# Optimization experiments

Measured on AMD Instinct MI355X. Metric: run time of the kernel, lower is better.

Reference implementation:

```python
import jax, jax.numpy as jnp
import numpy as np
from jax import lax

K_NEIGH = 20
BN_EPS = 1e-5


def conv2d(x, w, b, pad):
    # x: [B,C,H,W], w: [O,I,kh,kw]
    y = lax.conv_general_dilated(x, w, (1, 1), [(pad, pad), (pad, pad)],
                                 dimension_numbers=('NCHW', 'OIHW', 'NCHW'))
    return y + b[None, :, None, None]


def bn_train(h, gamma, beta):
    # h: [B,N,K,C]; BatchNorm1d in train mode: stats over (B,N,K) per channel
    mean = jnp.mean(h, axis=(0, 1, 2), keepdims=True)
    var = jnp.mean(jnp.square(h - mean), axis=(0, 1, 2), keepdims=True)
    return gamma * (h - mean) * lax.rsqrt(var + BN_EPS) + beta


def edge_conv(F1, w1, b1, g1, bt1, w2, b2, g2, bt2):
    # F1: [B,N,F] with F=1
    B, N, Fd = F1.shape
    sq = jnp.sum(F1 * F1, axis=-1)                               # [B,N]
    dist = sq[:, :, None] + sq[:, None, :] - 2.0 * jnp.einsum('bnf,bmf->bnm', F1, F1)
    idx = jnp.argsort(dist, axis=-1)[:, :, 1:K_NEIGH + 1]        # [B,N,K]
    knn = jax.vmap(lambda xb, ib: xb[ib])(F1, idx)               # [B,N,K,F]
    x1 = jnp.broadcast_to(F1[:, :, None, :], (B, N, K_NEIGH, Fd))
    x_in = jnp.concatenate([x1, knn - x1], axis=-1)              # [B,N,K,2F]
    h = jnp.einsum('bnkc,oc->bnko', x_in, w1) + b1               # 1x1 conv1d
    h = jax.nn.relu(bn_train(h, g1, bt1))
    o = jnp.einsum('bnkc,oc->bnko', h, w2) + b2
    o = jax.nn.relu(bn_train(o, g2, bt2))
    return jnp.max(o, axis=2)                                    # [B,N,an]


def pixel_shuffle(x, r):
    B, C, H, W = x.shape
    x = x.reshape(B, C // (r * r), r, r, H, W)
    x = x.transpose(0, 1, 4, 2, 5, 3)
    return x.reshape(B, C // (r * r), H * r, W * r)


def setup_inputs() -> dict:
    key = jax.random.key(0)
    ks = jax.random.split(key, 8)
    B, H, W = 4, 64, 64
    inp = {
        'x':   jax.random.normal(ks[0], (B, 1, H, W), jnp.float32),
        'c1w': jax.random.normal(ks[1], (64, 1, 5, 5), jnp.float32) * 0.1,
        'c1b': jnp.zeros((64,), jnp.float32),
        'c2w': jax.random.normal(ks[2], (32, 64, 3, 3), jnp.float32) * 0.05,
        'c2b': jnp.zeros((32,), jnp.float32),
        'c3w': jax.random.normal(ks[3], (16, 32, 3, 3), jnp.float32) * 0.05,
        'c3b': jnp.zeros((16,), jnp.float32),
        'c4w': jax.random.normal(ks[4], (1, 16, 3, 3), jnp.float32) * 0.05,
        'c4b': jnp.zeros((1,), jnp.float32),
        'ew1': jax.random.normal(ks[5], (3, 16, 2), jnp.float32) * 0.5,
        'eb1': jnp.zeros((3, 16), jnp.float32),
        'eg1': jnp.ones((3, 16), jnp.float32),
        'ebt1': jnp.zeros((3, 16), jnp.float32),
        'ew2': jax.random.normal(ks[6], (3, 1, 16), jnp.float32) * 0.25,
        'eb2': jnp.zeros((3, 1), jnp.float32),
        'eg2': jnp.ones((3, 1), jnp.float32),
        'ebt2': jnp.zeros((3, 1), jnp.float32),
    }
    return inp


def reference(x, c1w, c1b, c2w, c2b, c3w, c3b, c4w, c4b,
              ew1, eb1, eg1, ebt1, ew2, eb2, eg2, ebt2):
    h = jnp.tanh(conv2d(x, c1w, c1b, 2))
    h = jnp.tanh(conv2d(h, c2w, c2b, 1))
    h = jnp.tanh(conv2d(h, c3w, c3b, 1))
    h = conv2d(h, c4w, c4b, 1)                     # [B,1,H,W]
    B, C, H, W = h.shape
    F1 = h.reshape(B, C, H * W).transpose(0, 2, 1)  # [B,N,1]
    branches = [h]
    for i in range(3):
        o = edge_conv(F1, ew1[i], eb1[i], eg1[i], ebt1[i],
                      ew2[i], eb2[i], eg2[i], ebt2[i])  # [B,N,1]
        branches.append(o.transpose(0, 2, 1).reshape(B, C, H, W))
    p = jnp.concatenate(branches, axis=1)          # [B,4,H,W]
    return jax.nn.sigmoid(pixel_shuffle(p, 2))     # [B,1,2H,2W]
```

## Files before the change

### kernel.cpp

```cpp
#include <hip/hip_runtime.h>
#include <math.h>

#define NPIX 4096
#define KN 20
#define MTOT 327680.0

__device__ inline unsigned long long shflx64(unsigned long long v, int m) {
  unsigned lo = (unsigned)v, hi = (unsigned)(v >> 32);
  lo = __shfl_xor(lo, m, 64);
  hi = __shfl_xor(hi, m, 64);
  return (((unsigned long long)hi) << 32) | lo;
}

__global__ __launch_bounds__(512) void conv12_k(const float* __restrict__ x,
    const float* __restrict__ c1w, const float* __restrict__ c1b,
    const float* __restrict__ c2w, const float* __restrict__ c2b,
    float* __restrict__ part12) {
  __shared__ float sx[506];
  __shared__ float sc1[5472];
  const int tid = threadIdx.x;
  const int b = blockIdx.x, tile = blockIdx.y, z = blockIdx.z;
  const int th = (tile >> 2) << 4, tw = (tile & 3) << 4;

  for (int i = tid; i < 484; i += 512) {
    int r = i / 22, c = i - r*22;
    int gr = th - 3 + r, gc = tw - 3 + c;
    sx[r*23 + c] = (gr>=0 && gr<64 && gc>=0 && gc<64) ? x[b*NPIX + (gr<<6) + gc] : 0.f;
  }
  __syncthreads();
  for (int idx = tid; idx < 5184; idx += 512) {
    int co = idx / 324, rem = idx - co*324;
    int i = rem / 18, j = rem - i*18;
    int gy = th - 1 + i, gx = tw - 1 + j;
    bool inb = (gy>=0 && gy<64 && gx>=0 && gx<64);
    int cg = (z << 4) + co;
    float acc = c1b[cg];
#pragma unroll
    for (int di=0; di<5; di++)
#pragma unroll
      for (int dj=0; dj<5; dj++)
        acc = fmaf(sx[(i+di)*23 + j+dj], c1w[cg*25 + di*5 + dj], acc);
    sc1[co*342 + i*19 + j] = inb ? tanhf(acc) : 0.f;
  }
  __syncthreads();
  {
    const int l = tid & 63;
    const int w = __builtin_amdgcn_readfirstlane(tid >> 6);
    int row0 = (l >> 4) << 2;
    int col  = l & 15;
    int co0 = w << 2;
    float acc[16];
#pragma unroll
    for (int p=0;p<4;p++)
#pragma unroll
      for (int q=0;q<4;q++)
        acc[p*4+q] = (z == 0) ? c2b[co0+q] : 0.f;
#pragma unroll 2
    for (int ci = 0; ci < 16; ci++) {
      const float* sp = sc1 + ci*342;
      float vb[6][3];
#pragma unroll
      for (int r=0;r<6;r++)
#pragma unroll
        for (int dj=0;dj<3;dj++)
          vb[r][dj] = sp[(row0+r)*19 + col + dj];
      int cin = (z << 4) + ci;
#pragma unroll
      for (int q=0;q<4;q++) {
        const float* wq = c2w + ((size_t)(co0+q)*64 + cin)*9;
#pragma unroll
        for (int p=0;p<4;p++) {
          float a = acc[p*4+q];
#pragma unroll
          for (int di=0;di<3;di++)
#pragma unroll
            for (int dj=0;dj<3;dj++)
              a = fmaf(vb[p+di][dj], wq[di*3+dj], a);
          acc[p*4+q] = a;
        }
      }
    }
#pragma unroll
    for (int q=0;q<4;q++)
#pragma unroll
      for (int p=0;p<4;p++)
        part12[(((size_t)(z*4 + b)*32 + co0+q) << 12)
               + ((th+row0+p)<<6) + tw + col] = acc[p*4+q];
  }
}

__global__ __launch_bounds__(512) void conv34_k(const float* __restrict__ part12,
    const float* __restrict__ c3w, const float* __restrict__ c3b,
    const float* __restrict__ c4w, const float* __restrict__ c4b,
    float* __restrict__ fbuf) {
  __shared__ float sc2[3328];
  __shared__ float sc3[1248];
  __shared__ float red[1200];
  const int tid = threadIdx.x;
  const int b = blockIdx.x, tile = blockIdx.y;
  const int th = (tile >> 3) << 2, tw = (tile & 7) << 3;
  const int px = tid & 127;
  const int cinw = __builtin_amdgcn_readfirstlane(tid >> 7);

  for (int i = tid; i < 3072; i += 512) {
    int cin = i / 96, rem = i - cin*96;
    int rr = rem / 12, cc = rem - rr*12;
    int gr = th - 2 + rr, gc = tw - 2 + cc;
    float v = 0.f;
    if (gr>=0 && gr<64 && gc>=0 && gc<64) {
      size_t idx = (((size_t)b*32 + cin) << 12) + (gr<<6) + gc;
      v = tanhf(part12[idx] + part12[idx + 524288] +
                part12[idx + 1048576] + part12[idx + 1572864]);
    }
    sc2[cin*104 + rr*13 + cc] = v;
  }
  __syncthreads();
  float acc[16];
  int pi = px / 10, pj = px - pi*10;
  if (px < 60) {
#pragma unroll
    for (int o=0;o<16;o++) acc[o] = (cinw == 0) ? c3b[o] : 0.f;
    for (int ci = 0; ci < 8; ci++) {
      int cin = (cinw << 3) + ci;
      const float* sp = sc2 + cin*104;
      float v[9];
#pragma unroll
      for (int di=0;di<3;di++)
#pragma unroll
        for (int dj=0;dj<3;dj++)
          v[di*3+dj] = sp[(pi+di)*13 + pj+dj];
      const float* wc = c3w + cin*9;
#pragma unroll
      for (int o=0;o<16;o++) {
        const float* wo = wc + o*288;
#pragma unroll
        for (int t=0;t<9;t++)
          acc[o] = fmaf(v[t], wo[t], acc[o]);
      }
    }
  }
  int gy = th - 1 + pi, gx = tw - 1 + pj;
  bool inb = (gy>=0 && gy<64 && gx>=0 && gx<64);
  for (int ch = 0; ch < 4; ch++) {
    __syncthreads();
    if (px < 60) {
#pragma unroll
      for (int cc = 0; cc < 4; cc++)
        red[cinw*300 + px*5 + cc] = acc[(ch<<2) + cc];
    }
    __syncthreads();
    if (px < 60) {
      float s = red[0*300 + px*5 + cinw];
#pragma unroll
      for (int g=1; g<4; g++) s += red[g*300 + px*5 + cinw];
      int co = (ch<<2) + cinw;
      sc3[co*78 + pi*13 + pj] = inb ? tanhf(s) : 0.f;
    }
  }
  __syncthreads();
  if (tid < 32) {
    int py = tid >> 3, qx = tid & 7;
    float acc4 = c4b[0];
    for (int cin = 0; cin < 16; cin++) {
#pragma unroll
      for (int di=0;di<3;di++)
#pragma unroll
        for (int dj=0;dj<3;dj++)
          acc4 = fmaf(sc3[cin*78 + (py+di)*13 + qx+dj], c4w[cin*9 + di*3+dj], acc4);
    }
    fbuf[b*NPIX + ((th+py)<<6) + (tw+qx)] = acc4;
  }
}

__global__ __launch_bounds__(1024) void sort2_k(const float* __restrict__ f,
    float* __restrict__ sval, int* __restrict__ sidx) {
  int b = blockIdx.x;
  int tid = threadIdx.x;
  int l = tid & 63, w = tid >> 6;
  __shared__ unsigned long long Ab[NPIX];
  __shared__ unsigned long long Bb[NPIX];
  const float* fb = f + b*NPIX;
  unsigned long long key[4];
#pragma unroll
  for (int r=0;r<4;r++) {
    unsigned e = (w<<8) + (r<<6) + l;
    float v = fb[e];
    unsigned u = __float_as_uint(v);
    u ^= (u >> 31) ? 0xFFFFFFFFu : 0x80000000u;
    key[r] = (((unsigned long long)u) << 32) | e;
  }
  for (unsigned k = 2; k <= 256; k <<= 1) {
    for (unsigned j = k >> 1; j > 0; j >>= 1) {
      if (j >= 64) {
        unsigned rj = j >> 6;
#pragma unroll
        for (int r=0;r<4;r++) {
          int pr = r ^ (int)rj;
          if (pr > r) {
            unsigned e = (w<<8)+((unsigned)r<<6)+l;
            bool up = ((e & k & 255u) == 0);
            unsigned long long a = key[r], c = key[pr];
            bool sw = up ? (c < a) : (c > a);
            if (sw) { key[r] = c; key[pr] = a; }
          }
        }
      } else {
#pragma unroll
        for (int r=0;r<4;r++) {
          unsigned e = (w<<8)+((unsigned)r<<6)+l;
          unsigned long long a = key[r];
          unsigned long long p = shflx64(a, (int)j);
          bool up = ((e & k & 255u) == 0);
          bool keepmin = ((e & j) == 0) == up;
          key[r] = (keepmin ? (p < a) : (p > a)) ? p : a;
        }
      }
    }
  }
#pragma unroll
  for (int r=0;r<4;r++) Ab[(w<<8)+(r<<6)+l] = key[r];
  __syncthreads();
  unsigned long long* src = Ab;
  unsigned long long* dst = Bb;
  for (int lg = 8; lg <= 11; lg++) {
    const int L = 1 << lg;
    int p0 = tid << 2;
    int ri = p0 >> lg;
    int base = (ri ^ 1) << lg;
    int mbase = ((ri >> 1) << (lg + 1)) + (p0 & (L - 1));
    unsigned long long kk[4];
    int lo[4], hi[4];
#pragma unroll
    for (int r=0;r<4;r++) { kk[r] = src[p0 + r]; lo[r] = 0; hi[r] = L; }
    for (int s = 0; s <= lg; s++) {
#pragma unroll
      for (int r=0;r<4;r++) {
        if (lo[r] < hi[r]) {
          int mid = (lo[r] + hi[r]) >> 1;
          if (src[base + mid] < kk[r]) lo[r] = mid + 1; else hi[r] = mid;
        }
      }
    }
#pragma unroll
    for (int r=0;r<4;r++) dst[mbase + r + lo[r]] = kk[r];
    __syncthreads();
    unsigned long long* t = src; src = dst; dst = t;
  }
#pragma unroll
  for (int r=0;r<4;r++) {
    int p = (tid << 2) + r;
    unsigned long long kk = src[p];
    unsigned u = (unsigned)(kk >> 32);
    u ^= (u >> 31) ? 0x80000000u : 0xFFFFFFFFu;
    sval[b*NPIX + p] = __uint_as_float(u);
    sidx[b*NPIX + p] = (int)(kk & 0xFFFFFFFFu);
  }
}

__global__ __launch_bounds__(512) void knn4_k(const float* __restrict__ f,
    const float* __restrict__ sval, const int* __restrict__ sidx,
    float* __restrict__ dout, double* __restrict__ part1) {
  const int tid = threadIdx.x, blk = blockIdx.x;
  const int l = tid & 63, w = tid >> 6;
  const int bq = blk >> 7;
  const float* svb = sval + (bq << 12);
  const int*   sib = sidx + (bq << 12);
  const float* fB  = f + (bq << 12);
  double a0=0, a1=0, a2=0, a3=0, a4=0;
  unsigned long long kk[4];
  float fnp[4];
  int   sp[4];
#pragma unroll
  for (int p=0;p<4;p++) {
    int s = ((blk & 127) << 5) + (w << 2) + p;
    sp[p] = s;
    float fn = svb[s]; fnp[p] = fn;
    int start = s - 32;
    if (start < 0) start = 0;
    if (start > NPIX - 64) start = NPIX - 64;
    int q = start + l;
    float fm = svb[q];
    int   m  = sib[q];
    float sqn = __fmul_rn(fn, fn);
    float pr  = __fmul_rn(fn, fm);
    float dist = __fsub_rn(__fadd_rn(sqn, __fmul_rn(fm, fm)), __fmul_rn(2.0f, pr));
    unsigned u = __float_as_uint(dist);
    u ^= (u >> 31) ? 0xFFFFFFFFu : 0x80000000u;
    kk[p] = (((unsigned long long)u) << 32) | (unsigned)m;
  }
#pragma unroll
  for (int k = 2; k <= 64; k <<= 1)
#pragma unroll
    for (int j = k >> 1; j > 0; j >>= 1) {
#pragma unroll
      for (int p=0;p<4;p++) {
        unsigned long long pp = shflx64(kk[p], j);
        bool up = ((l & k) == 0);
        bool keepmin = ((l & j) == 0) == up;
        kk[p] = (keepmin ? (pp < kk[p]) : (pp > kk[p])) ? pp : kk[p];
      }
    }
#pragma unroll
  for (int p=0;p<4;p++) {
    int mr = (int)(kk[p] & 0xFFFFFFFFu);
    float fn = fnp[p];
    float d = __fsub_rn(fB[mr], fn);
    int n = sib[sp[p]];
    if (l >= 1 && l <= 20)
      dout[(size_t)((bq<<12) + n)*KN + (l-1)] = d;
    float dm = (l >= 1 && l <= 20) ? d : 0.f;
    a2 += (double)dm;
    a3 += (double)dm * (double)dm;
    a4 += (double)fn * (double)dm;
    if (l == 0) { a0 += (double)fn; a1 += (double)fn * (double)fn; }
  }
  double v[5] = {a0, a1, a2, a3, a4};
#pragma unroll
  for (int qi=0; qi<5; qi++)
    for (int off=32; off>0; off>>=1) v[qi] += __shfl_down(v[qi], off, 64);
  __shared__ double sred[8][5];
  if (l == 0)
#pragma unroll
    for (int qi=0; qi<5; qi++) sred[w][qi] = v[qi];
  __syncthreads();
  if (tid == 0) {
#pragma unroll
    for (int qi=0; qi<5; qi++) {
      double s = 0.0;
#pragma unroll
      for (int ww=0; ww<8; ww++) s += sred[ww][qi];
      part1[blk*5 + qi] = s;
    }
  }
}

__global__ __launch_bounds__(64) void branch_k(const float* __restrict__ f,
    const float* __restrict__ dw, const double* __restrict__ part1,
    const float* __restrict__ ew1, const float* __restrict__ eb1,
    const float* __restrict__ eg1, const float* __restrict__ ebt1,
    const float* __restrict__ ew2, const float* __restrict__ eb2,
    float* __restrict__ maxo, float* __restrict__ mino,
    double* __restrict__ part2) {
  const int l = threadIdx.x;
  const int blk = blockIdx.x, br = blockIdx.y;
  double a[5] = {0,0,0,0,0};
  for (int b2 = l; b2 < 512; b2 += 64)
#pragma unroll
    for (int q=0;q<5;q++) a[q] += part1[b2*5+q];
#pragma unroll
  for (int q=0;q<5;q++)
    for (int off=32; off>0; off>>=1) a[q] += __shfl_down(a[q], off, 64);
#pragma unroll
  for (int q=0;q<5;q++) a[q] = __shfl(a[q], 0, 64);
  double Ef = a[0]/16384.0, Eff = a[1]/16384.0;
  double Ed = a[2]/MTOT, Edd = a[3]/MTOT, Efd = a[4]/MTOT;
  double Vf = Eff - Ef*Ef, Vd = Edd - Ed*Ed, Cfd = Efd - Ef*Ed;
  float sA[16], sB[16], sC[16], sW[16];
#pragma unroll
  for (int c=0;c<16;c++) {
    int idx = br*16 + c;
    double w0 = (double)ew1[idx*2+0], w1 = (double)ew1[idx*2+1];
    double b1 = (double)eb1[idx];
    double m1 = w0*Ef + w1*Ed + b1;
    double v1 = w0*w0*Vf + 2.0*w0*w1*Cfd + w1*w1*Vd;
    double r1 = 1.0 / sqrt(v1 + 1e-5);
    double g = (double)eg1[idx];
    sA[c] = (float)(g*r1*w0);
    sB[c] = (float)(g*r1*w1);
    sC[c] = (float)(g*r1*(b1 - m1) + (double)ebt1[idx]);
    sW[c] = ew2[idx];
  }
  int row = (blk << 6) + l;
  float fv = f[row];
  const float* dd = dw + (size_t)row*KN;
  float b2v = eb2[br];
  float P[16];
#pragma unroll
  for (int c=0;c<16;c++) P[c] = fmaf(sA[c], fv, sC[c]);
  float mx = -INFINITY, mn = INFINITY;
  double s = 0.0, s2 = 0.0;
  for (int k=0;k<KN;k++) {
    float d = dd[k];
    float t = b2v;
#pragma unroll
    for (int c=0;c<16;c++)
      t = fmaf(sW[c], fmaxf(fmaf(sB[c], d, P[c]), 0.f), t);
    mx = fmaxf(mx, t);
    mn = fminf(mn, t);
    double td = (double)t;
    s += td; s2 += td*td;
  }
  maxo[br*16384 + row] = mx;
  mino[br*16384 + row] = mn;
#pragma unroll
  for (int off=32; off>0; off>>=1) {
    s  += __shfl_down(s, off, 64);
    s2 += __shfl_down(s2, off, 64);
  }
  if (l == 0) {
    part2[(br*256 + blk)*2 + 0] = s;
    part2[(br*256 + blk)*2 + 1] = s2;
  }
}

__global__ __launch_bounds__(256) void out_k(const float* __restrict__ f,
    const float* __restrict__ maxo, const float* __restrict__ mino,
    const double* __restrict__ part2,
    const float* __restrict__ eg2, const float* __restrict__ ebt2,
    float* __restrict__ out) {
  __shared__ float c2c[3][2];
  const int tid = threadIdx.x, blk = blockIdx.x;
  const int l = tid & 63, w = tid >> 6;
  if (w < 3) {
    int br = w;
    double s = 0.0, s2 = 0.0;
#pragma unroll
    for (int i=0;i<4;i++) {
      int bb = l + (i << 6);
      s  += part2[(br*256 + bb)*2 + 0];
      s2 += part2[(br*256 + bb)*2 + 1];
    }
#pragma unroll
    for (int off=32; off>0; off>>=1) {
      s  += __shfl_down(s, off, 64);
      s2 += __shfl_down(s2, off, 64);
    }
    if (l == 0) {
      double mean = s / MTOT;
      double var = s2 / MTOT - mean*mean;
      double r2 = 1.0 / sqrt(var + 1e-5);
      double sc = (double)eg2[br] * r2;
      c2c[br][0] = (float)sc;
      c2c[br][1] = (float)((double)ebt2[br] - sc*mean);
    }
  }
  __syncthreads();
  int tg = (blk << 8) + tid;
  int bo = tg >> 14;
  int y = (tg >> 7) & 127, xx = tg & 127;
  int n = ((y>>1)<<6) + (xx>>1);
  int ch = ((y&1)<<1) + (xx&1);
  float v;
  if (ch == 0) {
    v = f[bo*NPIX + n];
  } else {
    int br = ch - 1;
    float sc = c2c[br][0], sh = c2c[br][1];
    float base = (sc >= 0.f) ? maxo[br*16384 + bo*NPIX + n]
                             : mino[br*16384 + bo*NPIX + n];
    v = fmaxf(fmaf(sc, base, sh), 0.f);
  }
  out[tg] = 1.f / (1.f + expf(-v));
}

extern "C" void kernel_launch(void* const* d_in, const int* in_sizes, int n_in,
                              void* d_out, int out_size, void* d_ws, size_t ws_size,
                              hipStream_t stream) {
  (void)in_sizes; (void)n_in; (void)out_size; (void)ws_size;
  const float* x    = (const float*)d_in[0];
  const float* c1w  = (const float*)d_in[1];
  const float* c1b  = (const float*)d_in[2];
  const float* c2w  = (const float*)d_in[3];
  const float* c2b  = (const float*)d_in[4];
  const float* c3w  = (const float*)d_in[5];
  const float* c3b  = (const float*)d_in[6];
  const float* c4w  = (const float*)d_in[7];
  const float* c4b  = (const float*)d_in[8];
  const float* ew1  = (const float*)d_in[9];
  const float* eb1  = (const float*)d_in[10];
  const float* eg1  = (const float*)d_in[11];
  const float* ebt1 = (const float*)d_in[12];
  const float* ew2  = (const float*)d_in[13];
  const float* eb2  = (const float*)d_in[14];
  const float* eg2  = (const float*)d_in[15];
  const float* ebt2 = (const float*)d_in[16];
  float* out = (float*)d_out;
  float* ws  = (float*)d_ws;

  float*  part12 = ws;
  float*  fbuf  = ws + 2097152;
  float*  dw    = ws + 2113536;
  float*  sval  = ws + 2441216;
  int*    sidx  = (int*)(ws + 2457600);
  float*  maxo  = ws + 2473984;
  float*  mino  = ws + 2523136;
  double* part1 = (double*)(ws + 2572288);
  double* part2 = (double*)(ws + 2577408);

  conv12_k<<<dim3(4,16,4), 512, 0, stream>>>(x, c1w, c1b, c2w, c2b, part12);
  conv34_k<<<dim3(4,128), 512, 0, stream>>>(part12, c3w, c3b, c4w, c4b, fbuf);
  sort2_k<<<4, 1024, 0, stream>>>(fbuf, sval, sidx);
  knn4_k<<<512, 512, 0, stream>>>(fbuf, sval, sidx, dw, part1);
  branch_k<<<dim3(256,3), 64, 0, stream>>>(fbuf, dw, part1,
      ew1, eb1, eg1, ebt1, ew2, eb2, maxo, mino, part2);
  out_k<<<256, 256, 0, stream>>>(fbuf, maxo, mino, part2, eg2, ebt2, out);
}
```

Before: 104.6 us.

## Enlarge conv34 tiles to 8x8 and split conv3 by output channels

The conv3+conv4 kernel now handles 8x8 output tiles instead of 4x8, which halves the grid and shrinks the relative halo overhead, so fewer redundant tanh-of-sum loads from part12 are needed. Each of the four wave groups now computes four output channels over all 32 input channels, instead of splitting the input channels and reducing 16 partial sums through shared memory. This removes the reduction buffer and its repeated barriers. In exchange each thread runs a longer serial loop over channels, and the block count drops to 256, which lowers parallelism.

```diff
diff --git a/kernel.cpp b/kernel.cpp
--- a/kernel.cpp
+++ b/kernel.cpp
@@ -93,17 +93,16 @@
     const float* __restrict__ c3w, const float* __restrict__ c3b,
     const float* __restrict__ c4w, const float* __restrict__ c4b,
     float* __restrict__ fbuf) {
-  __shared__ float sc2[3328];
-  __shared__ float sc3[1248];
-  __shared__ float red[1200];
+  __shared__ float sc2[4992];
+  __shared__ float sc3[2080];
   const int tid = threadIdx.x;
   const int b = blockIdx.x, tile = blockIdx.y;
-  const int th = (tile >> 3) << 2, tw = (tile & 7) << 3;
+  const int th = (tile >> 3) << 3, tw = (tile & 7) << 3;
   const int px = tid & 127;
-  const int cinw = __builtin_amdgcn_readfirstlane(tid >> 7);
-
-  for (int i = tid; i < 3072; i += 512) {
-    int cin = i / 96, rem = i - cin*96;
+  const int coutg = __builtin_amdgcn_readfirstlane(tid >> 7);
+
+  for (int i = tid; i < 4608; i += 512) {
+    int cin = i / 144, rem = i - cin*144;
     int rr = rem / 12, cc = rem - rr*12;
     int gr = th - 2 + rr, gc = tw - 2 + cc;
     float v = 0.f;
@@ -112,17 +111,15 @@
       v = tanhf(part12[idx] + part12[idx + 524288] +
                 part12[idx + 1048576] + part12[idx + 1572864]);
     }
-    sc2[cin*104 + rr*13 + cc] = v;
-  }
-  __syncthreads();
-  float acc[16];
-  int pi = px / 10, pj = px - pi*10;
-  if (px < 60) {
-#pragma unroll
-    for (int o=0;o<16;o++) acc[o] = (cinw == 0) ? c3b[o] : 0.f;
-    for (int ci = 0; ci < 8; ci++) {
-      int cin = (cinw << 3) + ci;
-      const float* sp = sc2 + cin*104;
+    sc2[cin*156 + rr*13 + cc] = v;
+  }
+  __syncthreads();
+  if (px < 100) {
+    int pi = px / 10, pj = px - pi*10;
+    int co0 = coutg << 2;
+    float a0 = c3b[co0+0], a1 = c3b[co0+1], a2 = c3b[co0+2], a3 = c3b[co0+3];
+    for (int cin = 0; cin < 32; cin++) {
+      const float* sp = sc2 + cin*156;
       float v[9];
 #pragma unroll
       for (int di=0;di<3;di++)
@@ -130,35 +127,27 @@
         for (int dj=0;dj<3;dj++)
           v[di*3+dj] = sp[(pi+di)*13 + pj+dj];
       const float* wc = c3w + cin*9;
-#pragma unroll
-      for (int o=0;o<16;o++) {
-        const float* wo = wc + o*288;
-#pragma unroll
-        for (int t=0;t<9;t++)
-          acc[o] = fmaf(v[t], wo[t], acc[o]);
+      const float* w0p = wc + (size_t)(co0+0)*288;
+      const float* w1p = wc + (size_t)(co0+1)*288;
+      const float* w2p = wc + (size_t)(co0+2)*288;
+      const float* w3p = wc + (size_t)(co0+3)*288;
+#pragma unroll
+      for (int t=0;t<9;t++) {
+        a0 = fmaf(v[t], w0p[t], a0);
+        a1 = fmaf(v[t], w1p[t], a1);
+        a2 = fmaf(v[t], w2p[t], a2);
+        a3 = fmaf(v[t], w3p[t], a3);
       }
     }
-  }
-  int gy = th - 1 + pi, gx = tw - 1 + pj;
-  bool inb = (gy>=0 && gy<64 && gx>=0 && gx<64);
-  for (int ch = 0; ch < 4; ch++) {
-    __syncthreads();
-    if (px < 60) {
-#pragma unroll
-      for (int cc = 0; cc < 4; cc++)
-        red[cinw*300 + px*5 + cc] = acc[(ch<<2) + cc];
-    }
-    __syncthreads();
-    if (px < 60) {
-      float s = red[0*300 + px*5 + cinw];
-#pragma unroll
-      for (int g=1; g<4; g++) s += red[g*300 + px*5 + cinw];
-      int co = (ch<<2) + cinw;
-      sc3[co*78 + pi*13 + pj] = inb ? tanhf(s) : 0.f;
-    }
-  }
-  __syncthreads();
-  if (tid < 32) {
+    int gy = th - 1 + pi, gx = tw - 1 + pj;
+    bool inb = (gy>=0 && gy<64 && gx>=0 && gx<64);
+    sc3[(co0+0)*130 + pi*13 + pj] = inb ? tanhf(a0) : 0.f;
+    sc3[(co0+1)*130 + pi*13 + pj] = inb ? tanhf(a1) : 0.f;
+    sc3[(co0+2)*130 + pi*13 + pj] = inb ? tanhf(a2) : 0.f;
+    sc3[(co0+3)*130 + pi*13 + pj] = inb ? tanhf(a3) : 0.f;
+  }
+  __syncthreads();
+  if (tid < 64) {
     int py = tid >> 3, qx = tid & 7;
     float acc4 = c4b[0];
     for (int cin = 0; cin < 16; cin++) {
@@ -166,7 +155,7 @@
       for (int di=0;di<3;di++)
 #pragma unroll
         for (int dj=0;dj<3;dj++)
-          acc4 = fmaf(sc3[cin*78 + (py+di)*13 + qx+dj], c4w[cin*9 + di*3+dj], acc4);
+          acc4 = fmaf(sc3[cin*130 + (py+di)*13 + qx+dj], c4w[cin*9 + di*3+dj], acc4);
     }
     fbuf[b*NPIX + ((th+py)<<6) + (tw+qx)] = acc4;
   }
@@ -488,7 +477,7 @@
   double* part2 = (double*)(ws + 2577408);
 
   conv12_k<<<dim3(4,16,4), 512, 0, stream>>>(x, c1w, c1b, c2w, c2b, part12);
-  conv34_k<<<dim3(4,128), 512, 0, stream>>>(part12, c3w, c3b, c4w, c4b, fbuf);
+  conv34_k<<<dim3(4,64), 512, 0, stream>>>(part12, c3w, c3b, c4w, c4b, fbuf);
   sort2_k<<<4, 1024, 0, stream>>>(fbuf, sval, sidx);
   knn4_k<<<512, 512, 0, stream>>>(fbuf, sval, sidx, dw, part1);
   branch_k<<<dim3(256,3), 64, 0, stream>>>(fbuf, dw, part1,
```

New measurement: 104.3 us. No clear change (-0.2%).
